# Performance work log

Measured on AMD Instinct MI355X. Metric: run time of the kernel, lower is better.

The kernel has to match this reference:

```python
import jax, jax.numpy as jnp
import numpy as np

B, T, E, H, G = 8, 1024, 1024, 16, 4
D = E // H
SCALING = D ** -0.5
READER_W = 0.1  # reader_group_weight


def _heads(x):
    # [B, T, E] -> [B, H, T, D]
    return x.reshape(B, T, H, D).transpose(0, 2, 1, 3)


def setup_inputs() -> dict:
    key = jax.random.key(0)
    ks = jax.random.split(key, 16)
    s = 0.02
    return {
        "hidden_states": jax.random.normal(ks[0], (B, T, E), jnp.float32),
        "reader_token": jax.random.randint(ks[1], (B,), 0, G, dtype=jnp.int32),
        # shared (generic) projections, torch Linear convention: y = x @ W.T + b
        "Wq": jax.random.normal(ks[2], (E, E), jnp.float32) * s,
        "bq": jnp.zeros((E,), jnp.float32),
        "Wk": jax.random.normal(ks[3], (E, E), jnp.float32) * s,
        "bk": jnp.zeros((E,), jnp.float32),
        "Wv": jax.random.normal(ks[4], (E, E), jnp.float32) * s,
        "bv": jnp.zeros((E,), jnp.float32),
        "Wo": jax.random.normal(ks[5], (E, E), jnp.float32) * s,
        "bo": jnp.zeros((E,), jnp.float32),
        # stacked per-reader-group expert projections [G, E, E]
        "RWq": jax.random.normal(ks[6], (G, E, E), jnp.float32) * s,
        "Rbq": jnp.zeros((G, E), jnp.float32),
        "RWk": jax.random.normal(ks[7], (G, E, E), jnp.float32) * s,
        "Rbk": jnp.zeros((G, E), jnp.float32),
        "RWv": jax.random.normal(ks[8], (G, E, E), jnp.float32) * s,
        "Rbv": jnp.zeros((G, E), jnp.float32),
    }


def reference(hidden_states, reader_token, Wq, bq, Wk, bk, Wv, bv, Wo, bo,
              RWq, Rbq, RWk, Rbk, RWv, Rbv):
    hs = hidden_states
    # --- generic attention probs (shared weights) ---
    q = _heads((hs @ Wq.T + bq) * SCALING)          # [B,H,T,D]
    k = _heads(hs @ Wk.T + bk)                       # [B,H,T,D]
    v = _heads(hs @ Wv.T + bv)                       # [B,H,T,D]
    gen_probs = jax.nn.softmax(jnp.einsum('bhtd,bhsd->bhts', q, k), axis=-1)
    # --- reader-group attention probs (per-sample routed weights) ---
    Wq_b = RWq[reader_token]                          # [B,E,E]
    Wk_b = RWk[reader_token]
    q_r = _heads((jnp.einsum('bte,boe->bto', hs, Wq_b) + Rbq[reader_token][:, None, :]) * SCALING)
    k_r = _heads(jnp.einsum('bte,boe->bto', hs, Wk_b) + Rbk[reader_token][:, None, :])
    rdr_probs = jax.nn.softmax(jnp.einsum('bhtd,bhsd->bhts', q_r, k_r), axis=-1)
    # --- weighted combine, then attend over GENERIC value states ---
    probs = (READER_W * rdr_probs + (1.0 - READER_W) * gen_probs) / 2.0
    attn = jnp.einsum('bhts,bhsd->bhtd', probs, v)    # [B,H,T,D]
    attn = attn.transpose(0, 2, 1, 3).reshape(B, T, E)
    return attn @ Wo.T + bo
```

## Files before the change

kernel.cpp:

```cpp
#include <hip/hip_runtime.h>
#include <stdint.h>

#define AS1 __attribute__((address_space(1)))
#define AS3 __attribute__((address_space(3)))

typedef __attribute__((ext_vector_type(8))) short bf16x8;
typedef __attribute__((ext_vector_type(4))) float f32x4;

#define NB 8
#define NT 1024
#define NE 1024
#define NH 16
#define BT (NB * NT)

__device__ __forceinline__ unsigned short f2bf(float f) {
    unsigned int u = __builtin_bit_cast(unsigned int, f);
    u += 0x7FFFu + ((u >> 16) & 1u);
    return (unsigned short)(u >> 16);
}
__device__ __forceinline__ unsigned int cvt_pk_bf16(float lo, float hi) {
    unsigned int r;
    asm("v_cvt_pk_bf16_f32 %0, %1, %2" : "=v"(r) : "v"(lo), "v"(hi));
    return r;
}

__global__ void k_cvt7(const float* __restrict__ hs, unsigned short* __restrict__ hsB,
                       const float* __restrict__ w1, unsigned short* __restrict__ w1B,
                       const float* __restrict__ w2, unsigned short* __restrict__ w2B,
                       const float* __restrict__ w3, unsigned short* __restrict__ w3B,
                       const float* __restrict__ w4, unsigned short* __restrict__ w4B,
                       const float* __restrict__ r1, unsigned short* __restrict__ r1B,
                       const float* __restrict__ r2, unsigned short* __restrict__ r2B)
{
    int blk = blockIdx.x;
    const float* s; unsigned short* d; int base;
    if      (blk < 8192)  { s = hs; d = hsB; base = 0; }
    else if (blk < 9216)  { s = w1; d = w1B; base = 8192; }
    else if (blk < 10240) { s = w2; d = w2B; base = 9216; }
    else if (blk < 11264) { s = w3; d = w3B; base = 10240; }
    else if (blk < 12288) { s = w4; d = w4B; base = 11264; }
    else if (blk < 16384) { s = r1; d = r1B; base = 12288; }
    else                  { s = r2; d = r2B; base = 16384; }
    int i = ((blk - base) * 256 + threadIdx.x) * 4;
    float4 f = *reinterpret_cast<const float4*>(s + i);
    ushort4 o;
    o.x = f2bf(f.x); o.y = f2bf(f.y); o.z = f2bf(f.z); o.w = f2bf(f.w);
    *reinterpret_cast<ushort4*>(d + i) = o;
}

struct GJob {
    const unsigned short* W;
    const float* bias;
    void* out;
    float scale;
    int routed;
};

template <bool OUT_F32>
__global__ __launch_bounds__(256, 2)
void k_gemmP(const unsigned short* __restrict__ A,
             GJob j0, GJob j1, GJob j2, GJob j3, GJob j4,
             const int* __restrict__ rt)
{
    __shared__ __attribute__((aligned(16))) unsigned short LA[3][256 * 32];
    __shared__ __attribute__((aligned(16))) unsigned short LBb[3][128 * 32];

    const int flat = blockIdx.x;
    const int xcd = flat & 7;
    const int l   = flat >> 3;
    const int pz  = l >> 5;
    const int r   = l & 31;
    const int by  = xcd * 4 + (r >> 3);
    const int bx  = r & 7;
    const int m0 = by << 8, n0 = bx << 7;

    GJob jb = j0;
    if (pz == 1) jb = j1;
    else if (pz == 2) jb = j2;
    else if (pz == 3) jb = j3;
    else if (pz == 4) jb = j4;
    int g = jb.routed ? rt[m0 >> 10] : 0;
    const unsigned short* Wg = jb.W + (size_t)g * NE * NE;

    const int tid  = threadIdx.x;
    const int wid  = tid >> 6;
    const int lane = tid & 63;
    const int frow = lane & 15;
    const int g4   = lane >> 4;
    const int wm = wid >> 1, wn = wid & 1;

    const unsigned short* baseA = A  + (size_t)m0 * NE;
    const unsigned short* baseB = Wg + (size_t)n0 * NE;

    auto STAGE_A = [&](int buf, int kt) {
#pragma unroll
        for (int j = 0; j < 4; ++j) {
            int c = tid + j * 256;
            int row = c >> 2, cb = c & 3;
            const unsigned short* src = baseA + (size_t)row * NE + kt * 32
                                        + ((cb ^ ((row >> 1) & 3)) * 8);
            __builtin_amdgcn_global_load_lds((AS1 void*)src,
                (AS3 void*)(&LA[buf][0] + c * 8), 16, 0, 0);
        }
    };
    auto STAGE_B = [&](int buf, int kt) {
#pragma unroll
        for (int j = 0; j < 2; ++j) {
            int c = tid + j * 256;
            int row = c >> 2, cb = c & 3;
            const unsigned short* src = baseB + (size_t)row * NE + kt * 32
                                        + ((cb ^ ((row >> 1) & 3)) * 8);
            __builtin_amdgcn_global_load_lds((AS1 void*)src,
                (AS3 void*)(&LBb[buf][0] + c * 8), 16, 0, 0);
        }
    };

    f32x4 acc[8][4];
#pragma unroll
    for (int m = 0; m < 8; ++m)
#pragma unroll
        for (int n = 0; n < 4; ++n) acc[m][n] = (f32x4){0.f, 0.f, 0.f, 0.f};

    bf16x8 a4[4], b4[4];
    auto RDA = [&](int buf, int mh) {
#pragma unroll
        for (int mf = 0; mf < 4; ++mf) {
            int row = wm * 128 + mh * 64 + mf * 16 + frow;
            a4[mf] = *reinterpret_cast<const bf16x8*>(
                &LA[buf][row * 32 + ((g4 ^ ((row >> 1) & 3)) * 8)]);
        }
    };
    auto RDB = [&](int buf) {
#pragma unroll
        for (int nf = 0; nf < 4; ++nf) {
            int row = wn * 64 + nf * 16 + frow;
            b4[nf] = *reinterpret_cast<const bf16x8*>(
                &LBb[buf][row * 32 + ((g4 ^ ((row >> 1) & 3)) * 8)]);
        }
    };
    auto MM = [&](int mh) {
        __builtin_amdgcn_s_setprio(1);
#pragma unroll
        for (int mf = 0; mf < 4; ++mf)
#pragma unroll
            for (int nf = 0; nf < 4; ++nf)
                acc[mh * 4 + mf][nf] =
                    __builtin_amdgcn_mfma_f32_16x16x32_bf16(a4[mf], b4[nf], acc[mh * 4 + mf][nf], 0, 0, 0);
        __builtin_amdgcn_s_setprio(0);
    };

#define BARX __builtin_amdgcn_s_barrier()
#define LGK0 asm volatile("s_waitcnt lgkmcnt(0)" ::: "memory")
#define VMC6 asm volatile("s_waitcnt vmcnt(6)" ::: "memory")
#define VMC0 asm volatile("s_waitcnt vmcnt(0)" ::: "memory")

    STAGE_A(0, 0); STAGE_B(0, 0); STAGE_A(1, 1); STAGE_B(1, 1);
    VMC6; BARX;

    int bt = 0;
#pragma unroll 1
    for (int t = 0; t < 32; ++t) {
        const int b2 = (bt + 2 >= 3) ? bt - 1 : bt + 2;
        const bool pre = (t + 2 < 32);
        RDA(bt, 0); RDB(bt);
        if (pre) STAGE_A(b2, t + 2);
        BARX; LGK0; MM(0); BARX;
        RDA(bt, 1);
        if (pre) STAGE_B(b2, t + 2);
        BARX; LGK0; MM(1);
        if (t < 30) { VMC6; } else if (t == 30) { VMC0; }
        BARX;
        bt = (bt + 1 >= 3) ? 0 : bt + 1;
    }
#undef BARX
#undef LGK0
#undef VMC6
#undef VMC0

    const float* biasg = jb.bias + (size_t)g * NE;
#pragma unroll
    for (int am = 0; am < 8; ++am) {
        int row = m0 + wm * 128 + am * 16 + g4 * 4;
#pragma unroll
        for (int nf = 0; nf < 4; ++nf) {
            int col = n0 + wn * 64 + nf * 16 + frow;
            float bv = biasg[col];
            f32x4 v = acc[am][nf];
#pragma unroll
            for (int r2 = 0; r2 < 4; ++r2) {
                float val = (v[r2] + bv) * jb.scale;
                if (OUT_F32)
                    ((float*)jb.out)[(size_t)(row + r2) * NE + col] = val;
                else
                    ((unsigned short*)jb.out)[(size_t)(row + r2) * NE + col] = f2bf(val);
            }
        }
    }
}

__global__ void k_vtrans(const unsigned short* __restrict__ V, unsigned short* __restrict__ Vt) {
    __shared__ unsigned short tile[64][65];
    const int blk = blockIdx.x;
    const int bh = blk >> 4;
    const int b = bh >> 4;
    const int h = bh & 15;
    const int s0 = (blk & 15) * 64;
    const int tid = threadIdx.x;
#pragma unroll
    for (int i = 0; i < 2; ++i) {
        int seg = tid + i * 256;
        int row = seg >> 3;
        int c8 = (seg & 7) * 8;
        const unsigned short* src = V + (size_t)(b * NT + s0 + row) * NE + h * 64 + c8;
        ushort4 u0 = *reinterpret_cast<const ushort4*>(src);
        ushort4 u1 = *reinterpret_cast<const ushort4*>(src + 4);
        tile[row][c8 + 0] = u0.x; tile[row][c8 + 1] = u0.y;
        tile[row][c8 + 2] = u0.z; tile[row][c8 + 3] = u0.w;
        tile[row][c8 + 4] = u1.x; tile[row][c8 + 5] = u1.y;
        tile[row][c8 + 6] = u1.z; tile[row][c8 + 7] = u1.w;
    }
    __syncthreads();
#pragma unroll
    for (int i = 0; i < 2; ++i) {
        int seg = tid + i * 256;
        int drow = seg >> 3;
        int s8 = (seg & 7) * 8;
        ushort4 u0, u1;
        u0.x = tile[s8 + 0][drow]; u0.y = tile[s8 + 1][drow];
        u0.z = tile[s8 + 2][drow]; u0.w = tile[s8 + 3][drow];
        u1.x = tile[s8 + 4][drow]; u1.y = tile[s8 + 5][drow];
        u1.z = tile[s8 + 6][drow]; u1.w = tile[s8 + 7][drow];
        unsigned short* dst = Vt + (size_t)(bh * 64 + drow) * NT + s0 + s8;
        *reinterpret_cast<ushort4*>(dst) = u0;
        *reinterpret_cast<ushort4*>(dst + 4) = u1;
    }
}

__global__ __launch_bounds__(512, 4)
void k_attn(const unsigned short* __restrict__ Q,
            const unsigned short* __restrict__ K,
            const unsigned short* __restrict__ Qr,
            const unsigned short* __restrict__ Kr,
            const unsigned short* __restrict__ Vt,
            unsigned short* __restrict__ attnO)
{
    constexpr int PLD = 40;
    __shared__ __attribute__((aligned(16))) unsigned short KV[2][3 * 4096];
    __shared__ __attribute__((aligned(16))) unsigned short Pga[8][16 * PLD];
    __shared__ __attribute__((aligned(16))) unsigned short Pra[8][16 * PLD];

    const int blk = (blockIdx.x & 7) * 128 + (blockIdx.x >> 3);
    const int tile = blk & 7;
    const int bh = blk >> 3;
    const int b = bh >> 4;
    const int h = bh & 15;
    const int wid = threadIdx.x >> 6;
    const int lane = threadIdx.x & 63;
    const int frow = lane & 15;
    const int g4 = lane >> 4;
    const int f7 = frow & 7;
    const int fk8 = g4 * 8;
    const int t0 = tile * 128 + wid * 16;

    const size_t qoff = (size_t)(b * NT + t0 + frow) * NE + h * 64;
    const bf16x8 qf0 = *reinterpret_cast<const bf16x8*>(Q + qoff + fk8);
    const bf16x8 qf1 = *reinterpret_cast<const bf16x8*>(Q + qoff + 32 + fk8);
    const bf16x8 qr0 = *reinterpret_cast<const bf16x8*>(Qr + qoff + fk8);
    const bf16x8 qr1 = *reinterpret_cast<const bf16x8*>(Qr + qoff + 32 + fk8);

    const unsigned short* Kb  = K  + (size_t)b * NT * NE + h * 64;
    const unsigned short* Krb = Kr + (size_t)b * NT * NE + h * 64;
    const unsigned short* Vtb = Vt + (size_t)bh * 64 * NT;
    unsigned short* PgRow = &Pga[wid][0] + frow * PLD;
    unsigned short* PrRow = &Pra[wid][0] + frow * PLD;

    f32x4 og[4], orr[4];
    float lgp = 0.f, lrp = 0.f;
#pragma unroll
    for (int i = 0; i < 4; ++i) {
        og[i] = (f32x4){0.f, 0.f, 0.f, 0.f};
        orr[i] = (f32x4){0.f, 0.f, 0.f, 0.f};
    }

    const int srow = threadIdx.x >> 3;
    const int scb8 = ((threadIdx.x & 7) ^ (srow & 7)) * 8;
    auto stage = [&](int buf, int s0) {
        const unsigned short* sK = Kb  + (size_t)(s0 + srow) * NE + scb8;
        const unsigned short* sR = Krb + (size_t)(s0 + srow) * NE + scb8;
        const unsigned short* sV = Vtb + (size_t)srow * NT + s0 + scb8;
        __builtin_amdgcn_global_load_lds((AS1 void*)sK, (AS3 void*)(&KV[buf][wid * 512]), 16, 0, 0);
        __builtin_amdgcn_global_load_lds((AS1 void*)sR, (AS3 void*)(&KV[buf][4096 + wid * 512]), 16, 0, 0);
        __builtin_amdgcn_global_load_lds((AS1 void*)sV, (AS3 void*)(&KV[buf][8192 + wid * 512]), 16, 0, 0);
    };

    stage(0, 0);
    __syncthreads();
    int cur = 0;
    const f32x4 z = (f32x4){0.f, 0.f, 0.f, 0.f};
#pragma unroll 1
    for (int t = 0; t < NT / 64; ++t) {
        if (t < NT / 64 - 1) stage(cur ^ 1, (t + 1) * 64);
        const unsigned short* Kl  = &KV[cur][0];
        const unsigned short* Krl = &KV[cur][4096];
        const unsigned short* Vl  = &KV[cur][8192];

        f32x4 sg[4], sr[4];
#pragma unroll
        for (int nf = 0; nf < 4; ++nf) {
            const int ro = (nf * 16 + frow) * 64;
            bf16x8 kA = *reinterpret_cast<const bf16x8*>(Kl + ro + ((g4 ^ f7) * 8));
            bf16x8 kB = *reinterpret_cast<const bf16x8*>(Kl + ro + (((4 + g4) ^ f7) * 8));
            bf16x8 rA = *reinterpret_cast<const bf16x8*>(Krl + ro + ((g4 ^ f7) * 8));
            bf16x8 rB = *reinterpret_cast<const bf16x8*>(Krl + ro + (((4 + g4) ^ f7) * 8));
            sg[nf] = __builtin_amdgcn_mfma_f32_16x16x32_bf16(kA, qf0, z, 0, 0, 0);
            sg[nf] = __builtin_amdgcn_mfma_f32_16x16x32_bf16(kB, qf1, sg[nf], 0, 0, 0);
            sr[nf] = __builtin_amdgcn_mfma_f32_16x16x32_bf16(rA, qr0, z, 0, 0, 0);
            sr[nf] = __builtin_amdgcn_mfma_f32_16x16x32_bf16(rB, qr1, sr[nf], 0, 0, 0);
        }

#pragma unroll
        for (int hh = 0; hh < 2; ++hh) {
#pragma unroll
            for (int j = 0; j < 2; ++j) {
                const int nf = 2 * hh + j;
                float g0 = __expf(sg[nf][0]), g1 = __expf(sg[nf][1]);
                float g2 = __expf(sg[nf][2]), g3 = __expf(sg[nf][3]);
                lgp += (g0 + g1) + (g2 + g3);
                uint2 wg;
                wg.x = cvt_pk_bf16(g0, g1);
                wg.y = cvt_pk_bf16(g2, g3);
                *reinterpret_cast<uint2*>(PgRow + j * 16 + g4 * 4) = wg;
                float r0 = __expf(sr[nf][0]), r1 = __expf(sr[nf][1]);
                float r2 = __expf(sr[nf][2]), r3 = __expf(sr[nf][3]);
                lrp += (r0 + r1) + (r2 + r3);
                uint2 wr;
                wr.x = cvt_pk_bf16(r0, r1);
                wr.y = cvt_pk_bf16(r2, r3);
                *reinterpret_cast<uint2*>(PrRow + j * 16 + g4 * 4) = wr;
            }
            asm volatile("s_waitcnt lgkmcnt(0)" ::: "memory");
            bf16x8 pg = *reinterpret_cast<const bf16x8*>(PgRow + fk8);
            bf16x8 pr = *reinterpret_cast<const bf16x8*>(PrRow + fk8);
            __builtin_amdgcn_s_setprio(1);
#pragma unroll
            for (int nf2 = 0; nf2 < 4; ++nf2) {
                const int vo = (nf2 * 16 + frow) * 64;
                bf16x8 v = *reinterpret_cast<const bf16x8*>(Vl + vo + (((4 * hh + g4) ^ f7) * 8));
                og[nf2]  = __builtin_amdgcn_mfma_f32_16x16x32_bf16(pg, v, og[nf2], 0, 0, 0);
                orr[nf2] = __builtin_amdgcn_mfma_f32_16x16x32_bf16(pr, v, orr[nf2], 0, 0, 0);
            }
            __builtin_amdgcn_s_setprio(0);
        }

        __syncthreads();
        cur ^= 1;
    }

    lgp += __shfl_xor(lgp, 16); lgp += __shfl_xor(lgp, 32);
    lrp += __shfl_xor(lrp, 16); lrp += __shfl_xor(lrp, 32);
    float ig = 0.45f / lgp, ir = 0.05f / lrp;
    float igr[4], irr[4];
#pragma unroll
    for (int r = 0; r < 4; ++r) {
        igr[r] = __shfl(ig, g4 * 4 + r);
        irr[r] = __shfl(ir, g4 * 4 + r);
    }
#pragma unroll
    for (int nf2 = 0; nf2 < 4; ++nf2) {
#pragma unroll
        for (int r = 0; r < 4; ++r) {
            float val = og[nf2][r] * igr[r] + orr[nf2][r] * irr[r];
            int tq = t0 + g4 * 4 + r;
            attnO[(size_t)(b * NT + tq) * NE + h * 64 + nf2 * 16 + frow] = f2bf(val);
        }
    }
}

extern "C" void kernel_launch(void* const* d_in, const int* in_sizes, int n_in,
                              void* d_out, int out_size, void* d_ws, size_t ws_size,
                              hipStream_t stream)
{
    const float* hs  = (const float*)d_in[0];
    const int*   rt  = (const int*)d_in[1];
    const float* Wq  = (const float*)d_in[2];
    const float* bq  = (const float*)d_in[3];
    const float* Wk  = (const float*)d_in[4];
    const float* bk  = (const float*)d_in[5];
    const float* Wv  = (const float*)d_in[6];
    const float* bv  = (const float*)d_in[7];
    const float* Wo  = (const float*)d_in[8];
    const float* bo  = (const float*)d_in[9];
    const float* RWq = (const float*)d_in[10];
    const float* Rbq = (const float*)d_in[11];
    const float* RWk = (const float*)d_in[12];
    const float* Rbk = (const float*)d_in[13];

    unsigned short* w = (unsigned short*)d_ws;
    const size_t NBT = (size_t)BT * NE;
    const size_t NW  = (size_t)NE * NE;
    unsigned short* hsB  = w; w += NBT;
    unsigned short* Qb   = w; w += NBT;
    unsigned short* Kb   = w; w += NBT;
    unsigned short* Vb   = w; w += NBT;
    unsigned short* Qrb  = w; w += NBT;
    unsigned short* Krb  = w; w += NBT;
    unsigned short* Vtb  = w; w += NBT;
    unsigned short* atb  = w; w += NBT;
    unsigned short* WqB  = w; w += NW;
    unsigned short* WkB  = w; w += NW;
    unsigned short* WvB  = w; w += NW;
    unsigned short* WoB  = w; w += NW;
    unsigned short* RWqB = w; w += 4 * NW;
    unsigned short* RWkB = w; w += 4 * NW;

    k_cvt7<<<dim3(20480), dim3(256), 0, stream>>>(hs, hsB, Wq, WqB, Wk, WkB, Wv, WvB,
                                                  Wo, WoB, RWq, RWqB, RWk, RWkB);

    GJob jq  = { WqB,  bq,  Qb,  0.125f, 0 };
    GJob jk  = { WkB,  bk,  Kb,  1.0f,   0 };
    GJob jv  = { WvB,  bv,  Vb,  1.0f,   0 };
    GJob jrq = { RWqB, Rbq, Qrb, 0.125f, 1 };
    GJob jrk = { RWkB, Rbk, Krb, 1.0f,   1 };
    k_gemmP<false><<<dim3(1280), dim3(256), 0, stream>>>(hsB, jq, jk, jv, jrq, jrk, rt);

    k_vtrans<<<dim3(NB * NH * 16), dim3(256), 0, stream>>>(Vb, Vtb);
    k_attn<<<dim3(NB * NH * 8), dim3(512), 0, stream>>>(Qb, Kb, Qrb, Krb, Vtb, atb);

    GJob jo = { WoB, bo, d_out, 1.0f, 0 };
    k_gemmP<true><<<dim3(256), dim3(256), 0, stream>>>(atb, jo, jo, jo, jo, jo, nullptr);
}
```

Before: 243.9 us.

## Restructure projection GEMM to 512 threads with K=64 stages and 8-way swizzle

Rewrites the projection GEMM kernel so each 256x128 block uses 8 waves of 64x64 sub-tiles instead of 4 waves of 128x64. Each K stage grows from 32 to 64, which halves the loop trip count and barrier count, and the LDS swizzle changes to an 8-chunk XOR pattern. The aim is more waves for latency hiding, fewer accumulator registers per thread, and less synchronisation per K. In exchange LDS use rises to about 144KB per block with one block per CU.

```diff
diff --git a/kernel.cpp b/kernel.cpp
--- a/kernel.cpp
+++ b/kernel.cpp
@@ -57,13 +57,13 @@
 };
 
 template <bool OUT_F32>
-__global__ __launch_bounds__(256, 2)
-void k_gemmP(const unsigned short* __restrict__ A,
+__global__ __launch_bounds__(512, 1)
+void k_gemmN(const unsigned short* __restrict__ A,
              GJob j0, GJob j1, GJob j2, GJob j3, GJob j4,
              const int* __restrict__ rt)
 {
-    __shared__ __attribute__((aligned(16))) unsigned short LA[3][256 * 32];
-    __shared__ __attribute__((aligned(16))) unsigned short LBb[3][128 * 32];
+    __shared__ __attribute__((aligned(16))) unsigned short LA[3][2][128 * 64];
+    __shared__ __attribute__((aligned(16))) unsigned short LBb[3][128 * 64];
 
     const int flat = blockIdx.x;
     const int xcd = flat & 7;
@@ -89,63 +89,61 @@
     const int g4   = lane >> 4;
     const int wm = wid >> 1, wn = wid & 1;
 
+    const int rh0  = tid >> 3;
+    const int swz8 = ((tid & 7) ^ (rh0 & 7)) * 8;
     const unsigned short* baseA = A  + (size_t)m0 * NE;
     const unsigned short* baseB = Wg + (size_t)n0 * NE;
 
-    auto STAGE_A = [&](int buf, int kt) {
-#pragma unroll
-        for (int j = 0; j < 4; ++j) {
-            int c = tid + j * 256;
-            int row = c >> 2, cb = c & 3;
-            const unsigned short* src = baseA + (size_t)row * NE + kt * 32
-                                        + ((cb ^ ((row >> 1) & 3)) * 8);
+    auto STAGE_A = [&](int d, int half, int kt) {
+#pragma unroll
+        for (int j = 0; j < 2; ++j) {
+            const unsigned short* src =
+                baseA + (size_t)(half * 128 + rh0 + j * 64) * NE + kt * 64 + swz8;
             __builtin_amdgcn_global_load_lds((AS1 void*)src,
-                (AS3 void*)(&LA[buf][0] + c * 8), 16, 0, 0);
-        }
-    };
-    auto STAGE_B = [&](int buf, int kt) {
+                (AS3 void*)&LA[d][half][(tid + j * 512) * 8], 16, 0, 0);
+        }
+    };
+    auto STAGE_B = [&](int d, int kt) {
 #pragma unroll
         for (int j = 0; j < 2; ++j) {
-            int c = tid + j * 256;
-            int row = c >> 2, cb = c & 3;
-            const unsigned short* src = baseB + (size_t)row * NE + kt * 32
-                                        + ((cb ^ ((row >> 1) & 3)) * 8);
+            const unsigned short* src =
+                baseB + (size_t)(rh0 + j * 64) * NE + kt * 64 + swz8;
             __builtin_amdgcn_global_load_lds((AS1 void*)src,
-                (AS3 void*)(&LBb[buf][0] + c * 8), 16, 0, 0);
-        }
-    };
-
-    f32x4 acc[8][4];
-#pragma unroll
-    for (int m = 0; m < 8; ++m)
+                (AS3 void*)&LBb[d][(tid + j * 512) * 8], 16, 0, 0);
+        }
+    };
+
+    f32x4 acc[4][4];
+#pragma unroll
+    for (int m = 0; m < 4; ++m)
 #pragma unroll
         for (int n = 0; n < 4; ++n) acc[m][n] = (f32x4){0.f, 0.f, 0.f, 0.f};
 
     bf16x8 a4[4], b4[4];
-    auto RDA = [&](int buf, int mh) {
+    auto RDA = [&](int d, int kh) {
 #pragma unroll
         for (int mf = 0; mf < 4; ++mf) {
-            int row = wm * 128 + mh * 64 + mf * 16 + frow;
-            a4[mf] = *reinterpret_cast<const bf16x8*>(
-                &LA[buf][row * 32 + ((g4 ^ ((row >> 1) & 3)) * 8)]);
-        }
-    };
-    auto RDB = [&](int buf) {
+            int rowin = (wm & 1) * 64 + mf * 16 + frow;
+            int off = rowin * 64 + (((kh * 4 + g4) ^ (frow & 7)) * 8);
+            a4[mf] = *reinterpret_cast<const bf16x8*>(&LA[d][wm >> 1][off]);
+        }
+    };
+    auto RDB = [&](int d, int kh) {
 #pragma unroll
         for (int nf = 0; nf < 4; ++nf) {
-            int row = wn * 64 + nf * 16 + frow;
-            b4[nf] = *reinterpret_cast<const bf16x8*>(
-                &LBb[buf][row * 32 + ((g4 ^ ((row >> 1) & 3)) * 8)]);
-        }
-    };
-    auto MM = [&](int mh) {
+            int rowin = wn * 64 + nf * 16 + frow;
+            int off = rowin * 64 + (((kh * 4 + g4) ^ (frow & 7)) * 8);
+            b4[nf] = *reinterpret_cast<const bf16x8*>(&LBb[d][off]);
+        }
+    };
+    auto MM = [&]() {
         __builtin_amdgcn_s_setprio(1);
 #pragma unroll
         for (int mf = 0; mf < 4; ++mf)
 #pragma unroll
             for (int nf = 0; nf < 4; ++nf)
-                acc[mh * 4 + mf][nf] =
-                    __builtin_amdgcn_mfma_f32_16x16x32_bf16(a4[mf], b4[nf], acc[mh * 4 + mf][nf], 0, 0, 0);
+                acc[mf][nf] =
+                    __builtin_amdgcn_mfma_f32_16x16x32_bf16(a4[mf], b4[nf], acc[mf][nf], 0, 0, 0);
         __builtin_amdgcn_s_setprio(0);
     };
 
@@ -154,21 +152,22 @@
 #define VMC6 asm volatile("s_waitcnt vmcnt(6)" ::: "memory")
 #define VMC0 asm volatile("s_waitcnt vmcnt(0)" ::: "memory")
 
-    STAGE_A(0, 0); STAGE_B(0, 0); STAGE_A(1, 1); STAGE_B(1, 1);
+    STAGE_A(0, 0, 0); STAGE_A(0, 1, 0); STAGE_B(0, 0);
+    STAGE_A(1, 0, 1); STAGE_A(1, 1, 1); STAGE_B(1, 1);
     VMC6; BARX;
 
     int bt = 0;
 #pragma unroll 1
-    for (int t = 0; t < 32; ++t) {
+    for (int t = 0; t < 16; ++t) {
         const int b2 = (bt + 2 >= 3) ? bt - 1 : bt + 2;
-        const bool pre = (t + 2 < 32);
-        RDA(bt, 0); RDB(bt);
-        if (pre) STAGE_A(b2, t + 2);
-        BARX; LGK0; MM(0); BARX;
-        RDA(bt, 1);
-        if (pre) STAGE_B(b2, t + 2);
-        BARX; LGK0; MM(1);
-        if (t < 30) { VMC6; } else if (t == 30) { VMC0; }
+        const bool pre = (t + 2 < 16);
+        RDA(bt, 0); RDB(bt, 0);
+        if (pre) STAGE_A(b2, 0, t + 2);
+        BARX; LGK0; MM(); BARX;
+        RDA(bt, 1); RDB(bt, 1);
+        if (pre) { STAGE_A(b2, 1, t + 2); STAGE_B(b2, t + 2); }
+        BARX; LGK0; MM();
+        if (t < 14) { VMC6; } else if (t == 14) { VMC0; }
         BARX;
         bt = (bt + 1 >= 3) ? 0 : bt + 1;
     }
@@ -179,8 +178,8 @@
 
     const float* biasg = jb.bias + (size_t)g * NE;
 #pragma unroll
-    for (int am = 0; am < 8; ++am) {
-        int row = m0 + wm * 128 + am * 16 + g4 * 4;
+    for (int am = 0; am < 4; ++am) {
+        int row = m0 + wm * 64 + am * 16 + g4 * 4;
 #pragma unroll
         for (int nf = 0; nf < 4; ++nf) {
             int col = n0 + wn * 64 + nf * 16 + frow;
@@ -421,11 +420,11 @@
     GJob jv  = { WvB,  bv,  Vb,  1.0f,   0 };
     GJob jrq = { RWqB, Rbq, Qrb, 0.125f, 1 };
     GJob jrk = { RWkB, Rbk, Krb, 1.0f,   1 };
-    k_gemmP<false><<<dim3(1280), dim3(256), 0, stream>>>(hsB, jq, jk, jv, jrq, jrk, rt);
+    k_gemmN<false><<<dim3(1280), dim3(512), 0, stream>>>(hsB, jq, jk, jv, jrq, jrk, rt);
 
     k_vtrans<<<dim3(NB * NH * 16), dim3(256), 0, stream>>>(Vb, Vtb);
     k_attn<<<dim3(NB * NH * 8), dim3(512), 0, stream>>>(Qb, Kb, Qrb, Krb, Vtb, atb);
 
     GJob jo = { WoB, bo, d_out, 1.0f, 0 };
-    k_gemmP<true><<<dim3(256), dim3(256), 0, stream>>>(atb, jo, jo, jo, jo, jo, nullptr);
-}
+    k_gemmN<true><<<dim3(256), dim3(512), 0, stream>>>(atb, jo, jo, jo, jo, jo, nullptr);
+}
```

Measured after the change: 240.9 us. No clear change (-1.3%).
